# Optimization experiments

Measured on AMD Instinct MI355X. Metric: run time of the kernel, lower is better.

## Reference

```python
import jax, jax.numpy as jnp
import numpy as np

N = 131072   # total nodes in batch
D = 128      # hidden dim (in_dim = out_dim = 128)
DX = 64      # raw node feature dim (x and rw_feature each)
NG = 1024    # number of graphs (global_add_pool segments)
E = 4194304  # edges per hop adjacency (avg degree 32)
H = 4        # num_hops + 1 MLP branches per layer


def setup_inputs() -> dict:
    key = jax.random.key(0)
    ks = jax.random.split(key, 16)
    s = 0.05
    return {
        "x": jax.random.normal(ks[0], (N, DX), jnp.float32),
        "rw_feature": jax.random.normal(ks[1], (N, DX), jnp.float32),
        "hop1_features": jax.random.normal(ks[2], (N, D), jnp.float32),
        "hop2_features": jax.random.normal(ks[3], (N, D), jnp.float32),
        "hop3_features": jax.random.normal(ks[4], (N, D), jnp.float32),
        "hop1_edges": jax.random.randint(ks[5], (2, E), 0, N, dtype=jnp.int32),
        "hop2_edges": jax.random.randint(ks[6], (2, E), 0, N, dtype=jnp.int32),
        "hop3_edges": jax.random.randint(ks[7], (2, E), 0, N, dtype=jnp.int32),
        "batch": jnp.sort(jax.random.randint(ks[8], (N,), 0, NG, dtype=jnp.int32)),
        "l1_w1": jax.random.normal(ks[9], (H, D, D), jnp.float32) * s,
        "l1_b1": jnp.zeros((H, D), jnp.float32),
        "l1_w2": jax.random.normal(ks[10], (H, D, D), jnp.float32) * s,
        "l1_b2": jnp.zeros((H, D), jnp.float32),
        "l2_w1": jax.random.normal(ks[11], (H, D, D), jnp.float32) * s,
        "l2_b1": jnp.zeros((H, D), jnp.float32),
        "l2_w2": jax.random.normal(ks[12], (H, D, D), jnp.float32) * s,
        "l2_b2": jnp.zeros((H, D), jnp.float32),
        "lin_w": jax.random.normal(ks[13], (2 * D, D), jnp.float32) * s,
        "lin_b": jnp.zeros((D,), jnp.float32),
    }


def _mhc_layer(hops, w1, b1, w2, b2):
    # hops: [H, N, D]; per-hop MLP (Linear -> ReLU -> Dropout(eval) -> Linear), summed over hops
    z = jax.nn.relu(jnp.einsum('hni,hio->hno', hops, w1) + b1[:, None, :])
    y = jnp.einsum('hno,hop->hnp', z, w2) + b2[:, None, :]
    return jnp.sum(y, axis=0)  # [N, D]


def _spmm(edges, x):
    # torch.sparse.mm(A, x) with A[r, c] = 1.0 per edge; duplicate edges accumulate (COO sum)
    return jax.ops.segment_sum(x[edges[1]], edges[0], num_segments=N)


def reference(x, rw_feature, hop1_features, hop2_features, hop3_features,
              hop1_edges, hop2_edges, hop3_edges, batch,
              l1_w1, l1_b1, l1_w2, l1_b2, l2_w1, l2_b1, l2_w2, l2_b2,
              lin_w, lin_b):
    f = jnp.concatenate([x, rw_feature], axis=1)  # [N, D]
    h1 = jnp.stack([f, hop1_features, hop2_features, hop3_features], axis=0)  # [H, N, D]
    x1 = _mhc_layer(h1, l1_w1, l1_b1, l1_w2, l1_b2)
    h2 = jnp.stack([x1,
                    _spmm(hop1_edges, x1),
                    _spmm(hop2_edges, x1),
                    _spmm(hop3_edges, x1)], axis=0)
    x2 = _mhc_layer(h2, l2_w1, l2_b1, l2_w2, l2_b2)
    out = jnp.concatenate([x1, x2], axis=1) @ lin_w + lin_b  # concat=True path
    return jax.ops.segment_sum(out, batch, num_segments=NG)  # global_add_pool -> [NG, D]
```

## Files before the change

kernel.cpp:

```cpp
#include <hip/hip_runtime.h>

#define N_NODES 131072
#define DIM     128
#define NGRAPH  1024
#define NEDGE   4194304

#define NW      512
#define WBINS   256
#define NSL     512
#define SLICE_E (NEDGE / NSL)
#define CAP     12288

typedef float floatx4 __attribute__((ext_vector_type(4)));
typedef float f32x4  __attribute__((ext_vector_type(4)));
typedef __bf16 bf16x8 __attribute__((ext_vector_type(8)));
typedef __bf16 bf16x4 __attribute__((ext_vector_type(4)));

__device__ __forceinline__ int lds_off(int row, int kb) {
    return row * 256 + (kb ^ ((row & 7) << 4));
}

#define GLOAD16(gp, lp) __builtin_amdgcn_global_load_lds( \
    (const __attribute__((address_space(1))) void*)(gp),  \
    (__attribute__((address_space(3))) void*)(lp), 16, 0, 0)

__device__ __forceinline__ void stage_async(char* dstbase, const char* src,
                                            int w, int lane) {
#pragma unroll
    for (int it = 0; it < 8; ++it) {
        int chunk = it * 4 + w;
        int p = chunk * 1024 + lane * 16;
        int r = p >> 8;
        int o = p & 255;
        const char* g = src + r * 256 + (o ^ ((r & 7) << 4));
        GLOAD16(g, dstbase + chunk * 1024);
    }
}

__global__ __launch_bounds__(256)
void zero_kernel(floatx4* __restrict__ p, long n4) {
    long i = (long)blockIdx.x * blockDim.x + threadIdx.x;
    long stride = (long)gridDim.x * blockDim.x;
    floatx4 z = {0.f, 0.f, 0.f, 0.f};
    for (; i < n4; i += stride) p[i] = z;
}

__global__ __launch_bounds__(256)
void cvt_kernel(const float* __restrict__ src, __bf16* __restrict__ dst) {
    int i = blockIdx.x * 256 + threadIdx.x;
    const int stride = gridDim.x * 256;
    const int total = N_NODES * 32;
    for (; i < total; i += stride) {
        floatx4 v = ((const floatx4*)src)[i];
        bf16x4 h;
        h[0] = (__bf16)v[0]; h[1] = (__bf16)v[1];
        h[2] = (__bf16)v[2]; h[3] = (__bf16)v[3];
        ((bf16x4*)dst)[i] = h;
    }
}

__global__ __launch_bounds__(256)
void cvt_cat_kernel(const float* __restrict__ x, const float* __restrict__ rw,
                    __bf16* __restrict__ dst) {
    int i = blockIdx.x * 256 + threadIdx.x;
    const int stride = gridDim.x * 256;
    const int total = N_NODES * 32;
    for (; i < total; i += stride) {
        int rowg = i >> 5, g = i & 31;
        const float* s = (g < 16) ? x  + (size_t)rowg * 64 + g * 4
                                  : rw + (size_t)rowg * 64 + (g - 16) * 4;
        floatx4 v = *(const floatx4*)s;
        bf16x4 h;
        h[0] = (__bf16)v[0]; h[1] = (__bf16)v[1];
        h[2] = (__bf16)v[2]; h[3] = (__bf16)v[3];
        *(bf16x4*)(dst + (size_t)rowg * 128 + g * 4) = h;
    }
}

__global__ __launch_bounds__(256)
void tr_kernel(const float* __restrict__ src, __bf16* __restrict__ dst, int nmat) {
    int idx = blockIdx.x * blockDim.x + threadIdx.x;
    int total = nmat * 16384;
    if (idx >= total) return;
    int m = idx >> 14;
    int col = (idx >> 7) & 127;
    int k = idx & 127;
    dst[idx] = (__bf16)src[m * 16384 + k * 128 + col];
}

__global__ __launch_bounds__(256)
void wincount_kernel(const int* __restrict__ e1, const int* __restrict__ e2,
                     const int* __restrict__ e3, int* __restrict__ gcount) {
    const int gb = blockIdx.x;
    const int sl = gb % NSL;
    const int hop = gb / NSL;
    const int* rows = hop == 0 ? e1 : hop == 1 ? e2 : e3;

    __shared__ int cnt[NW];
    for (int i = threadIdx.x; i < NW; i += 256) cnt[i] = 0;
    __syncthreads();

    const int4* src = (const int4*)rows + (size_t)sl * (SLICE_E / 4);
    for (int j = threadIdx.x; j < SLICE_E / 4; j += 256) {
        int4 v = src[j];
        atomicAdd(&cnt[v.x >> 8], 1); atomicAdd(&cnt[v.y >> 8], 1);
        atomicAdd(&cnt[v.z >> 8], 1); atomicAdd(&cnt[v.w >> 8], 1);
    }
    __syncthreads();

    int* dst = gcount + ((size_t)hop * NSL + sl) * NW;
    for (int i = threadIdx.x; i < NW; i += 256) dst[i] = cnt[i];
}

__global__ __launch_bounds__(256)
void basescan_kernel(const int* __restrict__ gcount, int* __restrict__ baseo,
                     int* __restrict__ wbase) {
    const int hop = blockIdx.x;
    const int t = threadIdx.x;
    __shared__ int wt[NW];
    __shared__ int part[256];

    for (int k = 0; k < 2; ++k) {
        int w = t * 2 + k;
        int s = 0;
        for (int sl = 0; sl < NSL; ++sl)
            s += gcount[((size_t)hop * NSL + sl) * NW + w];
        wt[w] = s;
    }
    __syncthreads();
    part[t] = wt[2 * t] + wt[2 * t + 1];
    __syncthreads();
    for (int d = 1; d < 256; d <<= 1) {
        int v = (t >= d) ? part[t - d] : 0;
        __syncthreads();
        part[t] += v;
        __syncthreads();
    }
    int run = (t == 0) ? 0 : part[t - 1];
    for (int k = 0; k < 2; ++k) {
        int w = 2 * t + k;
        wbase[hop * (NW + 1) + w] = run;
        int r2 = run;
        for (int sl = 0; sl < NSL; ++sl) {
            baseo[((size_t)hop * NW + w) * NSL + sl] = r2;
            r2 += gcount[((size_t)hop * NSL + sl) * NW + w];
        }
        run += wt[w];
    }
    if (t == 255) wbase[hop * (NW + 1) + NW] = NEDGE;
}

__global__ __launch_bounds__(256)
void bucket_kernel(const int* __restrict__ e1, const int* __restrict__ e2,
                   const int* __restrict__ e3, const int* __restrict__ baseo,
                   int* __restrict__ buf) {
    const int gb = blockIdx.x;
    const int sl = gb % NSL;
    const int hop = gb / NSL;
    const int* rows = hop == 0 ? e1 : hop == 1 ? e2 : e3;
    const int* cs = rows + NEDGE;
    const int t = threadIdx.x;

    __shared__ int hist[NW];
    __shared__ int segstart[NW + 1];
    __shared__ int part[256];
    __shared__ int image[SLICE_E];

    for (int i = t; i < NW; i += 256) hist[i] = 0;
    __syncthreads();

    const int4* r4 = (const int4*)rows + (size_t)sl * (SLICE_E / 4);
    const int4* c4 = (const int4*)cs + (size_t)sl * (SLICE_E / 4);
    for (int j = t; j < SLICE_E / 4; j += 256) {
        int4 v = r4[j];
        atomicAdd(&hist[v.x >> 8], 1); atomicAdd(&hist[v.y >> 8], 1);
        atomicAdd(&hist[v.z >> 8], 1); atomicAdd(&hist[v.w >> 8], 1);
    }
    __syncthreads();

    int a = hist[2 * t], b = hist[2 * t + 1];
    part[t] = a + b;
    __syncthreads();
    for (int d = 1; d < 256; d <<= 1) {
        int v = (t >= d) ? part[t - d] : 0;
        __syncthreads();
        part[t] += v;
        __syncthreads();
    }
    int base = (t == 0) ? 0 : part[t - 1];
    segstart[2 * t] = base;
    segstart[2 * t + 1] = base + a;
    if (t == 255) segstart[NW] = SLICE_E;
    __syncthreads();
    hist[2 * t] = base;
    hist[2 * t + 1] = base + a;
    __syncthreads();

    for (int j = t; j < SLICE_E / 4; j += 256) {
        int4 r = r4[j];
        int4 c = c4[j];
        int p;
        p = atomicAdd(&hist[r.x >> 8], 1); image[p] = ((r.x & 255) << 17) | c.x;
        p = atomicAdd(&hist[r.y >> 8], 1); image[p] = ((r.y & 255) << 17) | c.y;
        p = atomicAdd(&hist[r.z >> 8], 1); image[p] = ((r.z & 255) << 17) | c.z;
        p = atomicAdd(&hist[r.w >> 8], 1); image[p] = ((r.w & 255) << 17) | c.w;
    }
    __syncthreads();

    int* bufh = buf + (size_t)hop * NEDGE;
    const int* bo = baseo + (size_t)hop * NW * NSL + sl;
    for (int j = t; j < SLICE_E; j += 256) {
        int lo = 0, hi = NW;
        while (hi - lo > 1) {
            int mid = (lo + hi) >> 1;
            if (segstart[mid] <= j) lo = mid; else hi = mid;
        }
        int dst = bo[(size_t)lo * NSL] + (j - segstart[lo]);
        bufh[dst] = image[j];
    }
}

__global__ __launch_bounds__(256)
void winbuild_kernel(const int* __restrict__ buf, const int* __restrict__ wbase,
                     int* __restrict__ offs3, int* __restrict__ cols) {
    const int gb = blockIdx.x;
    const int w = gb % NW;
    const int hop = gb / NW;
    const int b0 = wbase[hop * (NW + 1) + w];
    const int b1 = wbase[hop * (NW + 1) + w + 1];
    const int tot = b1 - b0;
    const int* src = buf + (size_t)hop * NEDGE + b0;
    int* col = cols + (size_t)hop * NEDGE;
    int* offs = offs3 + (size_t)hop * (N_NODES + 1);
    const int t = threadIdx.x;

    __shared__ int hist[WBINS];
    __shared__ int scanb[WBINS];
    __shared__ int image[CAP];

    hist[t] = 0;
    __syncthreads();
    for (int i = t; i < tot; i += 256) atomicAdd(&hist[src[i] >> 17], 1);
    __syncthreads();

    int v = hist[t];
    scanb[t] = v;
    __syncthreads();
    for (int d = 1; d < 256; d <<= 1) {
        int u = (t >= d) ? scanb[t - d] : 0;
        __syncthreads();
        scanb[t] += u;
        __syncthreads();
    }
    const int excl = scanb[t] - v;

    offs[w * WBINS + t] = b0 + excl;
    if (w == NW - 1 && t == 0) offs[N_NODES] = NEDGE;
    __syncthreads();

    if (tot <= CAP) {
        hist[t] = excl;
        __syncthreads();
        for (int i = t; i < tot; i += 256) {
            int e = src[i];
            int p = atomicAdd(&hist[e >> 17], 1);
            image[p] = e & 0x1FFFF;
        }
        __syncthreads();
        for (int i = t; i < tot; i += 256) col[b0 + i] = image[i];
    } else {
        hist[t] = b0 + excl;
        __syncthreads();
        for (int i = t; i < tot; i += 256) {
            int e = src[i];
            int p = atomicAdd(&hist[e >> 17], 1);
            col[p] = e & 0x1FFFF;
        }
    }
}

__global__ __launch_bounds__(256)
void csr_spmm_kernel(const int* __restrict__ offs, const int* __restrict__ col,
                     const __bf16* __restrict__ xin, __bf16* __restrict__ outb) {
    const int lane = threadIdx.x & 63;
    const int row = blockIdx.x * (blockDim.x >> 6) + (threadIdx.x >> 6);
    if (row >= N_NODES) return;
    const int beg = offs[row];
    const int end = offs[row + 1];

    float a0 = 0.f, a1 = 0.f, b0 = 0.f, b1 = 0.f;
    float c0f = 0.f, c1f = 0.f, d0 = 0.f, d1 = 0.f;
    for (int b = beg; b < end; b += 64) {
        const int n = min(64, end - b);
        int cidx = (b + lane < end) ? col[b + lane] : 0;
        int i = 0;
        for (; i + 4 <= n; i += 4) {
            int e0 = __shfl(cidx, i);
            int e1 = __shfl(cidx, i + 1);
            int e2 = __shfl(cidx, i + 2);
            int e3 = __shfl(cidx, i + 3);
            unsigned v0 = *(const unsigned*)(xin + (size_t)e0 * 128 + lane * 2);
            unsigned v1 = *(const unsigned*)(xin + (size_t)e1 * 128 + lane * 2);
            unsigned v2 = *(const unsigned*)(xin + (size_t)e2 * 128 + lane * 2);
            unsigned v3 = *(const unsigned*)(xin + (size_t)e3 * 128 + lane * 2);
            a0 += __uint_as_float(v0 << 16); a1 += __uint_as_float(v0 & 0xffff0000u);
            b0 += __uint_as_float(v1 << 16); b1 += __uint_as_float(v1 & 0xffff0000u);
            c0f += __uint_as_float(v2 << 16); c1f += __uint_as_float(v2 & 0xffff0000u);
            d0 += __uint_as_float(v3 << 16); d1 += __uint_as_float(v3 & 0xffff0000u);
        }
        for (; i < n; ++i) {
            int e = __shfl(cidx, i);
            unsigned v = *(const unsigned*)(xin + (size_t)e * 128 + lane * 2);
            a0 += __uint_as_float(v << 16); a1 += __uint_as_float(v & 0xffff0000u);
        }
    }
    float o0 = a0 + b0 + c0f + d0;
    float o1 = a1 + b1 + c1f + d1;
    union { unsigned u; __bf16 h[2]; } pk;
    pk.h[0] = (__bf16)o0; pk.h[1] = (__bf16)o1;
    *(unsigned*)(outb + (size_t)row * 128 + lane * 2) = pk.u;
}

__device__ __forceinline__ void mfma_relu_phase(char* az, const char* wb,
                                                const float* bias,
                                                int r0, int lrow, int grp) {
    bf16x8 am[2][4];
#pragma unroll
    for (int mt = 0; mt < 2; ++mt)
#pragma unroll
        for (int kk = 0; kk < 4; ++kk)
            am[mt][kk] = *(const bf16x8*)(az + lds_off(r0 + mt * 16 + lrow,
                                                       kk * 64 + grp * 16));
#pragma unroll
    for (int n = 0; n < 8; ++n) {
        f32x4 a0 = {0.f, 0.f, 0.f, 0.f};
        f32x4 a1 = {0.f, 0.f, 0.f, 0.f};
#pragma unroll
        for (int kk = 0; kk < 4; ++kk) {
            bf16x8 b = *(const bf16x8*)(wb + lds_off(n * 16 + lrow,
                                                     kk * 64 + grp * 16));
            a0 = __builtin_amdgcn_mfma_f32_16x16x32_bf16(am[0][kk], b, a0, 0, 0, 0);
            a1 = __builtin_amdgcn_mfma_f32_16x16x32_bf16(am[1][kk], b, a1, 0, 0, 0);
        }
        float bs = bias[n * 16 + lrow];
#pragma unroll
        for (int rg = 0; rg < 4; ++rg) {
            float v0 = fmaxf(a0[rg] + bs, 0.f);
            float v1 = fmaxf(a1[rg] + bs, 0.f);
            *(__bf16*)(az + lds_off(r0 + grp * 4 + rg, (n * 16 + lrow) * 2)) = (__bf16)v0;
            *(__bf16*)(az + lds_off(r0 + 16 + grp * 4 + rg, (n * 16 + lrow) * 2)) = (__bf16)v1;
        }
    }
}

__device__ __forceinline__ void mfma_phase(const char* az, const char* wb,
                                           int r0, int lrow, int grp,
                                           f32x4 (&acc)[2][8]) {
    bf16x8 am[2][4];
#pragma unroll
    for (int mt = 0; mt < 2; ++mt)
#pragma unroll
        for (int kk = 0; kk < 4; ++kk)
            am[mt][kk] = *(const bf16x8*)(az + lds_off(r0 + mt * 16 + lrow,
                                                       kk * 64 + grp * 16));
#pragma unroll
    for (int kk = 0; kk < 4; ++kk)
#pragma unroll
        for (int n = 0; n < 8; ++n) {
            bf16x8 b = *(const bf16x8*)(wb + lds_off(n * 16 + lrow,
                                                     kk * 64 + grp * 16));
#pragma unroll
            for (int mt = 0; mt < 2; ++mt)
                acc[mt][n] = __builtin_amdgcn_mfma_f32_16x16x32_bf16(
                    am[mt][kk], b, acc[mt][n], 0, 0, 0);
        }
}

__global__ __launch_bounds__(256, 2)
void layer1_kernel(const __bf16* __restrict__ xr, const __bf16* __restrict__ f1,
                   const __bf16* __restrict__ f2, const __bf16* __restrict__ f3,
                   const __bf16* __restrict__ wt1, const float* __restrict__ b1,
                   const __bf16* __restrict__ wt2, const float* __restrict__ b2,
                   __bf16* __restrict__ x1out)
{
    __shared__ uint4 lds_u4[4096];
    char* AZ = (char*)lds_u4;
    char* WB = (char*)lds_u4 + 32768;
    const int tid = threadIdx.x;
    const int lane = tid & 63;
    const int w = tid >> 6;
    const int r0 = w * 32;
    const int lrow = lane & 15;
    const int grp = lane >> 4;
    const int row0 = blockIdx.x * 128;

    f32x4 Y[2][8];
#pragma unroll
    for (int mt = 0; mt < 2; ++mt)
#pragma unroll
        for (int n = 0; n < 8; ++n) Y[mt][n] = {0.f, 0.f, 0.f, 0.f};

    for (int h = 0; h < 4; ++h) {
        const __bf16* feat = (h == 0) ? xr : (h == 1) ? f1 : (h == 2) ? f2 : f3;
        __syncthreads();
        stage_async(AZ, (const char*)(feat + (size_t)row0 * 128), w, lane);
        stage_async(WB, (const char*)(wt1 + (size_t)h * 16384), w, lane);
        __syncthreads();

        mfma_relu_phase(AZ, WB, b1 + h * 128, r0, lrow, grp);

        __syncthreads();
        stage_async(WB, (const char*)(wt2 + (size_t)h * 16384), w, lane);
        __syncthreads();
        mfma_phase(AZ, WB, r0, lrow, grp, Y);
    }

#pragma unroll
    for (int n = 0; n < 8; ++n) {
        int cc = n * 16 + lrow;
        float bs = b2[cc] + b2[128 + cc] + b2[256 + cc] + b2[384 + cc];
#pragma unroll
        for (int mt = 0; mt < 2; ++mt)
#pragma unroll
            for (int rg = 0; rg < 4; ++rg) {
                int zr = r0 + mt * 16 + grp * 4 + rg;
                *(__bf16*)(AZ + lds_off(zr, cc * 2)) = (__bf16)(Y[mt][n][rg] + bs);
            }
    }
    __syncthreads();
#pragma unroll
    for (int it = 0; it < 8; ++it) {
        int f = tid + it * 256;
        int r = f >> 4, o = f & 15;
        uint4 v = *(const uint4*)(AZ + lds_off(r, o * 16));
        *(uint4*)(x1out + (size_t)(row0 + r) * 128 + o * 8) = v;
    }
}

__global__ __launch_bounds__(256, 2)
void layer2_kernel(const __bf16* __restrict__ x1b, const __bf16* __restrict__ s1,
                   const __bf16* __restrict__ s2, const __bf16* __restrict__ s3,
                   const __bf16* __restrict__ wt1, const float* __restrict__ b1,
                   const __bf16* __restrict__ wt2, const float* __restrict__ b2,
                   const __bf16* __restrict__ wtl, const float* __restrict__ linb,
                   const int* __restrict__ batch, float* __restrict__ dout)
{
    __shared__ uint4 lds_u4[4096];
    char* AZ = (char*)lds_u4;
    char* WB = (char*)lds_u4 + 32768;
    const int tid = threadIdx.x;
    const int lane = tid & 63;
    const int w = tid >> 6;
    const int r0 = w * 32;
    const int lrow = lane & 15;
    const int grp = lane >> 4;
    const int row0 = blockIdx.x * 128;

    f32x4 Y[2][8];
#pragma unroll
    for (int mt = 0; mt < 2; ++mt)
#pragma unroll
        for (int n = 0; n < 8; ++n) Y[mt][n] = {0.f, 0.f, 0.f, 0.f};

    for (int h = 0; h < 4; ++h) {
        const __bf16* feat = (h == 0) ? x1b : (h == 1) ? s1 : (h == 2) ? s2 : s3;
        __syncthreads();
        stage_async(AZ, (const char*)(feat + (size_t)row0 * 128), w, lane);
        stage_async(WB, (const char*)(wt1 + (size_t)h * 16384), w, lane);
        __syncthreads();

        mfma_relu_phase(AZ, WB, b1 + h * 128, r0, lrow, grp);

        __syncthreads();
        stage_async(WB, (const char*)(wt2 + (size_t)h * 16384), w, lane);
        __syncthreads();
        mfma_phase(AZ, WB, r0, lrow, grp, Y);
    }

#pragma unroll
    for (int n = 0; n < 8; ++n) {
        int cc = n * 16 + lrow;
        float bs = b2[cc] + b2[128 + cc] + b2[256 + cc] + b2[384 + cc];
#pragma unroll
        for (int mt = 0; mt < 2; ++mt)
#pragma unroll
            for (int rg = 0; rg < 4; ++rg) {
                float v = Y[mt][n][rg] + bs;
                int zr = r0 + mt * 16 + grp * 4 + rg;
                *(__bf16*)(AZ + lds_off(zr, (n * 16 + lrow) * 2)) = (__bf16)v;
            }
    }
    __syncthreads();
    stage_async(WB, (const char*)(wtl + 16384), w, lane);
    __syncthreads();

    f32x4 o[2][8];
#pragma unroll
    for (int mt = 0; mt < 2; ++mt)
#pragma unroll
        for (int n = 0; n < 8; ++n) o[mt][n] = {0.f, 0.f, 0.f, 0.f};
    mfma_phase(AZ, WB, r0, lrow, grp, o);

    __syncthreads();
    stage_async(AZ, (const char*)(x1b + (size_t)row0 * 128), w, lane);
    stage_async(WB, (const char*)wtl, w, lane);
    __syncthreads();
    mfma_phase(AZ, WB, r0, lrow, grp, o);

    __syncthreads();
    float* tile32 = (float*)lds_u4;
#pragma unroll
    for (int n = 0; n < 8; ++n) {
        int cc = n * 16 + lrow;
        float lb = linb[cc];
#pragma unroll
        for (int mt = 0; mt < 2; ++mt)
#pragma unroll
            for (int rg = 0; rg < 4; ++rg) {
                int rl = r0 + mt * 16 + grp * 4 + rg;
                tile32[rl * 128 + cc] = o[mt][n][rg] + lb;
            }
    }
    __syncthreads();

    if (tid < 128) {
        const int d = tid;
        float acc = 0.f;
        int cur = batch[row0];
        for (int r = 0; r < 128; ++r) {
            int b = batch[row0 + r];
            if (b != cur) {
                atomicAdd(dout + (size_t)cur * 128 + d, acc);
                acc = 0.f;
                cur = b;
            }
            acc += tile32[r * 128 + d];
        }
        atomicAdd(dout + (size_t)cur * 128 + d, acc);
    }
}

extern "C" void kernel_launch(void* const* d_in, const int* in_sizes, int n_in,
                              void* d_out, int out_size, void* d_ws, size_t ws_size,
                              hipStream_t stream) {
    (void)in_sizes; (void)n_in; (void)out_size; (void)ws_size;

    const float* x    = (const float*)d_in[0];
    const float* rw   = (const float*)d_in[1];
    const float* f1   = (const float*)d_in[2];
    const float* f2   = (const float*)d_in[3];
    const float* f3   = (const float*)d_in[4];
    const int*   e1   = (const int*)d_in[5];
    const int*   e2   = (const int*)d_in[6];
    const int*   e3   = (const int*)d_in[7];
    const int*   batch= (const int*)d_in[8];
    const float* l1w1 = (const float*)d_in[9];
    const float* l1b1 = (const float*)d_in[10];
    const float* l1w2 = (const float*)d_in[11];
    const float* l1b2 = (const float*)d_in[12];
    const float* l2w1 = (const float*)d_in[13];
    const float* l2b1 = (const float*)d_in[14];
    const float* l2w2 = (const float*)d_in[15];
    const float* l2b2 = (const float*)d_in[16];
    const float* linw = (const float*)d_in[17];
    const float* linb = (const float*)d_in[18];

    float* out = (float*)d_out;

    __bf16* x1b = (__bf16*)d_ws;
    __bf16* s1b = x1b + (size_t)N_NODES * 128;
    __bf16* s2b = s1b + (size_t)N_NODES * 128;
    __bf16* s3b = s2b + (size_t)N_NODES * 128;
    __bf16* wt  = s3b + (size_t)N_NODES * 128;
    __bf16* wt_l1w1 = wt;
    __bf16* wt_l1w2 = wt + 4 * 16384;
    __bf16* wt_l2w1 = wt + 8 * 16384;
    __bf16* wt_l2w2 = wt + 12 * 16384;
    __bf16* wt_lin  = wt + 16 * 16384;
    int* ibase  = (int*)(wt + 18 * 16384);
    int* offs3  = ibase;
    int* gcount = offs3 + (size_t)3 * (N_NODES + 1);
    int* baseo  = gcount + (size_t)3 * NSL * NW;
    int* wbase  = baseo + (size_t)3 * NW * NSL;
    int* buf    = wbase + (size_t)3 * (NW + 1);
    int* cols   = buf + (size_t)3 * NEDGE;
    __bf16* xrb = (__bf16*)buf;

    tr_kernel<<<256, 256, 0, stream>>>(l1w1, wt_l1w1, 4);
    tr_kernel<<<256, 256, 0, stream>>>(l1w2, wt_l1w2, 4);
    tr_kernel<<<256, 256, 0, stream>>>(l2w1, wt_l2w1, 4);
    tr_kernel<<<256, 256, 0, stream>>>(l2w2, wt_l2w2, 4);
    tr_kernel<<<128, 256, 0, stream>>>(linw, wt_lin, 2);

    cvt_cat_kernel<<<4096, 256, 0, stream>>>(x, rw, xrb);
    cvt_kernel<<<4096, 256, 0, stream>>>(f1, s1b);
    cvt_kernel<<<4096, 256, 0, stream>>>(f2, s2b);
    cvt_kernel<<<4096, 256, 0, stream>>>(f3, s3b);

    zero_kernel<<<64, 256, 0, stream>>>((floatx4*)out, (long)NGRAPH * 32);

    layer1_kernel<<<N_NODES / 128, 256, 0, stream>>>(
        xrb, s1b, s2b, s3b, wt_l1w1, l1b1, wt_l1w2, l1b2, x1b);

    wincount_kernel<<<3 * NSL, 256, 0, stream>>>(e1, e2, e3, gcount);
    basescan_kernel<<<3, 256, 0, stream>>>(gcount, baseo, wbase);
    bucket_kernel<<<3 * NSL, 256, 0, stream>>>(e1, e2, e3, baseo, buf);
    winbuild_kernel<<<3 * NW, 256, 0, stream>>>(buf, wbase, offs3, cols);

    __bf16* ss[3] = {s1b, s2b, s3b};
    for (int hop = 0; hop < 3; ++hop) {
        csr_spmm_kernel<<<N_NODES / 4, 256, 0, stream>>>(
            offs3 + (size_t)hop * (N_NODES + 1), cols + (size_t)hop * NEDGE,
            x1b, ss[hop]);
    }

    layer2_kernel<<<N_NODES / 128, 256, 0, stream>>>(
        x1b, s1b, s2b, s3b, wt_l2w1, l2b1, wt_l2w2, l2b2, wt_lin, linb, batch, out);
}
```

Measured before the change: 908.9 us.

## Sub-bucket CSR columns by source range and sweep rows in column-phase order

The CSR build now splits each row's edges into 8 sub-buckets by source-node range and stores per-row byte counts. The SpMM kernel gives each wavefront 16 rows and walks them in 8 phases, touching only source rows in one range per phase. The aim is to keep the gathered x1 working set small enough to hit in cache, which cuts random HBM gathers. In exchange it adds a larger LDS histogram, an extra counts array, 8-bit counts that overflow if a row has more than 255 edges in one sub-bucket, and less parallelism per wave.

```diff
diff --git a/kernel.cpp b/kernel.cpp
--- a/kernel.cpp
+++ b/kernel.cpp
@@ -7,9 +7,12 @@
 
 #define NW      512
 #define WBINS   256
+#define NCW     8
+#define HBINS   (WBINS * NCW)
 #define NSL     512
 #define SLICE_E (NEDGE / NSL)
 #define CAP     12288
+#define SP_BATCH 16
 
 typedef float floatx4 __attribute__((ext_vector_type(4)));
 typedef float f32x4  __attribute__((ext_vector_type(4)));
@@ -222,7 +225,8 @@
 
 __global__ __launch_bounds__(256)
 void winbuild_kernel(const int* __restrict__ buf, const int* __restrict__ wbase,
-                     int* __restrict__ offs3, int* __restrict__ cols) {
+                     int* __restrict__ offs3, int* __restrict__ cols,
+                     uint2* __restrict__ cnts3) {
     const int gb = blockIdx.x;
     const int w = gb % NW;
     const int hop = gb / NW;
@@ -232,93 +236,124 @@
     const int* src = buf + (size_t)hop * NEDGE + b0;
     int* col = cols + (size_t)hop * NEDGE;
     int* offs = offs3 + (size_t)hop * (N_NODES + 1);
+    uint2* cnts = cnts3 + (size_t)hop * N_NODES;
     const int t = threadIdx.x;
 
-    __shared__ int hist[WBINS];
-    __shared__ int scanb[WBINS];
+    __shared__ int hist[HBINS];
+    __shared__ int part[256];
     __shared__ int image[CAP];
 
-    hist[t] = 0;
-    __syncthreads();
-    for (int i = t; i < tot; i += 256) atomicAdd(&hist[src[i] >> 17], 1);
-    __syncthreads();
-
-    int v = hist[t];
-    scanb[t] = v;
+#pragma unroll
+    for (int j = 0; j < NCW; ++j) hist[t * NCW + j] = 0;
+    __syncthreads();
+
+    for (int i = t; i < tot; i += 256) {
+        int e = src[i];
+        int key = ((e >> 17) << 3) | ((e & 0x1FFFF) >> 14);
+        atomicAdd(&hist[key], 1);
+    }
+    __syncthreads();
+
+    int loc[NCW];
+    int s = 0;
+#pragma unroll
+    for (int j = 0; j < NCW; ++j) { loc[j] = hist[t * NCW + j]; s += loc[j]; }
+    part[t] = s;
     __syncthreads();
     for (int d = 1; d < 256; d <<= 1) {
-        int u = (t >= d) ? scanb[t - d] : 0;
-        __syncthreads();
-        scanb[t] += u;
-        __syncthreads();
-    }
-    const int excl = scanb[t] - v;
+        int v = (t >= d) ? part[t - d] : 0;
+        __syncthreads();
+        part[t] += v;
+        __syncthreads();
+    }
+    const int excl = part[t] - s;
 
     offs[w * WBINS + t] = b0 + excl;
     if (w == NW - 1 && t == 0) offs[N_NODES] = NEDGE;
+
+    unsigned cx = 0, cy = 0;
+    int run = excl;
+#pragma unroll
+    for (int j = 0; j < NCW; ++j) {
+        if (j < 4) cx |= (unsigned)loc[j] << (8 * j);
+        else       cy |= (unsigned)loc[j] << (8 * (j - 4));
+        hist[t * NCW + j] = (tot <= CAP) ? run : b0 + run;
+        run += loc[j];
+    }
+    cnts[w * WBINS + t] = make_uint2(cx, cy);
     __syncthreads();
 
     if (tot <= CAP) {
-        hist[t] = excl;
-        __syncthreads();
         for (int i = t; i < tot; i += 256) {
             int e = src[i];
-            int p = atomicAdd(&hist[e >> 17], 1);
+            int key = ((e >> 17) << 3) | ((e & 0x1FFFF) >> 14);
+            int p = atomicAdd(&hist[key], 1);
             image[p] = e & 0x1FFFF;
         }
         __syncthreads();
         for (int i = t; i < tot; i += 256) col[b0 + i] = image[i];
     } else {
-        hist[t] = b0 + excl;
-        __syncthreads();
         for (int i = t; i < tot; i += 256) {
             int e = src[i];
-            int p = atomicAdd(&hist[e >> 17], 1);
+            int key = ((e >> 17) << 3) | ((e & 0x1FFFF) >> 14);
+            int p = atomicAdd(&hist[key], 1);
             col[p] = e & 0x1FFFF;
         }
     }
 }
 
 __global__ __launch_bounds__(256)
-void csr_spmm_kernel(const int* __restrict__ offs, const int* __restrict__ col,
+void csr_spmm_kernel(const int* __restrict__ offs,
+                     const unsigned char* __restrict__ cntb,
+                     const int* __restrict__ col,
                      const __bf16* __restrict__ xin, __bf16* __restrict__ outb) {
     const int lane = threadIdx.x & 63;
-    const int row = blockIdx.x * (blockDim.x >> 6) + (threadIdx.x >> 6);
-    if (row >= N_NODES) return;
-    const int beg = offs[row];
-    const int end = offs[row + 1];
-
-    float a0 = 0.f, a1 = 0.f, b0 = 0.f, b1 = 0.f;
-    float c0f = 0.f, c1f = 0.f, d0 = 0.f, d1 = 0.f;
-    for (int b = beg; b < end; b += 64) {
-        const int n = min(64, end - b);
-        int cidx = (b + lane < end) ? col[b + lane] : 0;
-        int i = 0;
-        for (; i + 4 <= n; i += 4) {
-            int e0 = __shfl(cidx, i);
-            int e1 = __shfl(cidx, i + 1);
-            int e2 = __shfl(cidx, i + 2);
-            int e3 = __shfl(cidx, i + 3);
-            unsigned v0 = *(const unsigned*)(xin + (size_t)e0 * 128 + lane * 2);
-            unsigned v1 = *(const unsigned*)(xin + (size_t)e1 * 128 + lane * 2);
-            unsigned v2 = *(const unsigned*)(xin + (size_t)e2 * 128 + lane * 2);
-            unsigned v3 = *(const unsigned*)(xin + (size_t)e3 * 128 + lane * 2);
-            a0 += __uint_as_float(v0 << 16); a1 += __uint_as_float(v0 & 0xffff0000u);
-            b0 += __uint_as_float(v1 << 16); b1 += __uint_as_float(v1 & 0xffff0000u);
-            c0f += __uint_as_float(v2 << 16); c1f += __uint_as_float(v2 & 0xffff0000u);
-            d0 += __uint_as_float(v3 << 16); d1 += __uint_as_float(v3 & 0xffff0000u);
-        }
-        for (; i < n; ++i) {
-            int e = __shfl(cidx, i);
-            unsigned v = *(const unsigned*)(xin + (size_t)e * 128 + lane * 2);
-            a0 += __uint_as_float(v << 16); a1 += __uint_as_float(v & 0xffff0000u);
-        }
-    }
-    float o0 = a0 + b0 + c0f + d0;
-    float o1 = a1 + b1 + c1f + d1;
-    union { unsigned u; __bf16 h[2]; } pk;
-    pk.h[0] = (__bf16)o0; pk.h[1] = (__bf16)o1;
-    *(unsigned*)(outb + (size_t)row * 128 + lane * 2) = pk.u;
+    const int wid = blockIdx.x * 4 + (threadIdx.x >> 6);
+    const int row0 = wid * SP_BATCH;
+
+    float a0[SP_BATCH], a1[SP_BATCH];
+    int cur[SP_BATCH];
+#pragma unroll
+    for (int r = 0; r < SP_BATCH; ++r) {
+        a0[r] = 0.f; a1[r] = 0.f;
+        cur[r] = offs[row0 + r];
+    }
+
+    for (int p = 0; p < NCW; ++p) {
+#pragma unroll 1
+        for (int r = 0; r < SP_BATCH; ++r) {
+            int len = cntb[(size_t)(row0 + r) * 8 + p];
+            while (len > 0) {
+                int n = min(len, 64);
+                int cidx = (lane < n) ? col[cur[r] + lane] : 0;
+                int i = 0;
+                for (; i + 2 <= n; i += 2) {
+                    int c0 = __shfl(cidx, i);
+                    int c1 = __shfl(cidx, i + 1);
+                    unsigned v0 = *(const unsigned*)(xin + (size_t)c0 * 128 + lane * 2);
+                    unsigned v1 = *(const unsigned*)(xin + (size_t)c1 * 128 + lane * 2);
+                    a0[r] += __uint_as_float(v0 << 16);
+                    a1[r] += __uint_as_float(v0 & 0xffff0000u);
+                    a0[r] += __uint_as_float(v1 << 16);
+                    a1[r] += __uint_as_float(v1 & 0xffff0000u);
+                }
+                for (; i < n; ++i) {
+                    int c = __shfl(cidx, i);
+                    unsigned v = *(const unsigned*)(xin + (size_t)c * 128 + lane * 2);
+                    a0[r] += __uint_as_float(v << 16);
+                    a1[r] += __uint_as_float(v & 0xffff0000u);
+                }
+                cur[r] += n; len -= n;
+            }
+        }
+    }
+
+#pragma unroll
+    for (int r = 0; r < SP_BATCH; ++r) {
+        union { unsigned u; __bf16 h[2]; } pk;
+        pk.h[0] = (__bf16)a0[r]; pk.h[1] = (__bf16)a1[r];
+        *(unsigned*)(outb + (size_t)(row0 + r) * 128 + lane * 2) = pk.u;
+    }
 }
 
 __device__ __forceinline__ void mfma_relu_phase(char* az, const char* wb,
@@ -584,6 +619,7 @@
     int* wbase  = baseo + (size_t)3 * NW * NSL;
     int* buf    = wbase + (size_t)3 * (NW + 1);
     int* cols   = buf + (size_t)3 * NEDGE;
+    uint2* cnts3 = (uint2*)(cols + (size_t)3 * NEDGE);
     __bf16* xrb = (__bf16*)buf;
 
     tr_kernel<<<256, 256, 0, stream>>>(l1w1, wt_l1w1, 4);
@@ -605,13 +641,14 @@
     wincount_kernel<<<3 * NSL, 256, 0, stream>>>(e1, e2, e3, gcount);
     basescan_kernel<<<3, 256, 0, stream>>>(gcount, baseo, wbase);
     bucket_kernel<<<3 * NSL, 256, 0, stream>>>(e1, e2, e3, baseo, buf);
-    winbuild_kernel<<<3 * NW, 256, 0, stream>>>(buf, wbase, offs3, cols);
+    winbuild_kernel<<<3 * NW, 256, 0, stream>>>(buf, wbase, offs3, cols, cnts3);
 
     __bf16* ss[3] = {s1b, s2b, s3b};
     for (int hop = 0; hop < 3; ++hop) {
-        csr_spmm_kernel<<<N_NODES / 4, 256, 0, stream>>>(
-            offs3 + (size_t)hop * (N_NODES + 1), cols + (size_t)hop * NEDGE,
-            x1b, ss[hop]);
+        csr_spmm_kernel<<<N_NODES / (4 * SP_BATCH), 256, 0, stream>>>(
+            offs3 + (size_t)hop * (N_NODES + 1),
+            (const unsigned char*)(cnts3 + (size_t)hop * N_NODES),
+            cols + (size_t)hop * NEDGE, x1b, ss[hop]);
     }
 
     layer2_kernel<<<N_NODES / 128, 256, 0, stream>>>(
```

Result: slower. 1.641 ms (+80.6%).
